# Kernel tuning notes

Measured on AMD Instinct MI355X. Metric: run time of the kernel, lower is better.

The kernel has to match this reference:

```python
import jax, jax.numpy as jnp
import numpy as np

T = 0.07          # cfg.CAP.TEMP
K = 50            # cfg.CAP.HARD_NEG_K
LOSS_WEIGHT = 0.5 # cfg.CAP.LOSS_WEIGHT
C_CAM = 8         # number of cameras
P = 2048          # pseudo-ID classes per camera bank


def setup_inputs() -> dict:
    key = jax.random.key(0)
    k1, k2, k3, k4 = jax.random.split(key, 4)
    B, D = 256, 2048
    inputs = jax.random.normal(k1, (B, D), jnp.float32)
    labels = jax.random.randint(k2, (B,), 0, P)
    cams = jax.random.randint(k3, (B,), 0, C_CAM)
    tempV = jax.random.normal(k4, (C_CAM * P, D), jnp.float32)
    tempV = tempV / jnp.linalg.norm(tempV, axis=1, keepdims=True)  # memory rows are L2-normalized
    return {"inputs": inputs, "labels": labels, "cams": cams, "tempV": tempV}


def _seg_mean_sum(vals, cams):
    # original loops over unique cams: loss += mean(vals within cam); empty cams contribute 0
    sums = jax.ops.segment_sum(vals, cams, num_segments=C_CAM)
    cnts = jax.ops.segment_sum(jnp.ones_like(vals), cams, num_segments=C_CAM)
    return jnp.sum(jnp.where(cnts > 0, sums / jnp.maximum(cnts, 1.0), 0.0))


def reference(inputs, labels, cams, tempV):
    B = inputs.shape[0]
    # cfg.CAP.NORM_FEAT
    x = inputs / jnp.linalg.norm(inputs, axis=1, keepdims=True)

    # one fused matmul against the concatenated memory; per-camera banks are contiguous P-slices
    all_logits = x @ tempV.T                      # [B, C_CAM*P]
    logits3 = all_logits.reshape(B, C_CAM, P)

    # ---- intra-camera loss: logits against the sample's own camera bank ----
    percam = jnp.take_along_axis(logits3, cams[:, None, None], axis=1)[:, 0, :] / T  # [B, P]
    lse_i = jax.scipy.special.logsumexp(percam, axis=1)
    ce = lse_i - jnp.take_along_axis(percam, labels[:, None], axis=1)[:, 0]
    loss_intra = _seg_mean_sum(ce, cams)

    # ---- inter-camera loss with hard-negative mining ----
    rows = jnp.arange(B)[:, None]
    # each ID has one centroid in every camera bank: positions label + P*cam
    ori_ind = labels[:, None] + P * jnp.arange(C_CAM)[None, :]        # [B, C_CAM]
    sims = all_logits.at[rows, ori_ind].set(-10000.0)                 # mask positives
    _, sel_ind = jax.lax.top_k(sims, K)                               # hard negatives (== sort[-K:])
    ori_logits = jnp.take_along_axis(all_logits, ori_ind, axis=1) / T  # [B, C_CAM]
    sel_logits = jnp.take_along_axis(all_logits, sel_ind, axis=1) / T  # [B, K]
    cat = jnp.concatenate([ori_logits, sel_logits], axis=1)            # [B, C_CAM+K]
    lse_c = jax.scipy.special.logsumexp(cat, axis=1)
    # target = 1/len(ori) on positives, 0 on negatives -> lse - mean(positive logits)
    loss_k = lse_c - jnp.mean(ori_logits, axis=1)
    loss_inter = LOSS_WEIGHT * _seg_mean_sum(loss_k, cams)

    return (loss_intra, loss_inter)
```

## Files before the change

kernel.cpp:

```cpp
#include <hip/hip_runtime.h>
#include <hip/hip_bf16.h>

#define BATCH 256
#define DIM   2048
#define NMEM  16384
#define PCLS  2048
#define CCAM  8
#define KSEL  50
#define T_INV 14.285714285714285714f
#define NB2   2048

typedef __bf16 bf16x8 __attribute__((ext_vector_type(8)));
typedef float  f32x4  __attribute__((ext_vector_type(4)));

static __device__ __forceinline__ unsigned int f2bf(float f) {
  unsigned int u = __float_as_uint(f);
  return (u + 0x7FFFu + ((u >> 16) & 1u)) >> 16;
}
static __device__ __forceinline__ unsigned int pk2(float lo, float hi) {
  return f2bf(lo) | (f2bf(hi) << 16);
}
static __device__ __forceinline__ int binw(float x, float lo, float scale) {
  int b = (int)((x - lo) * scale);
  return b > (NB2 - 1) ? (NB2 - 1) : b;
}

static __device__ __forceinline__ size_t pa_idx(int r, int c) {
  return (size_t)(r >> 4) * (size_t)(64 * 8 * (DIM / 32))
       + (size_t)(c >> 5) * 512
       + (size_t)(((r & 15) | (((c >> 3) & 3) << 4))) * 8
       + (size_t)(c & 7);
}

__global__ __launch_bounds__(256) void norm_cast_kernel(
    const float* __restrict__ in, unsigned short* __restrict__ xpk) {
  __shared__ float red[256];
  const int b = blockIdx.x, t = threadIdx.x;
  const float4* row = (const float4*)(in + (size_t)b * DIM);
  float4 a0 = row[t];
  float4 a1 = row[t + 256];
  float ss = a0.x*a0.x + a0.y*a0.y + a0.z*a0.z + a0.w*a0.w
           + a1.x*a1.x + a1.y*a1.y + a1.z*a1.z + a1.w*a1.w;
  red[t] = ss; __syncthreads();
  for (int s = 128; s > 0; s >>= 1) { if (t < s) red[t] += red[t + s]; __syncthreads(); }
  const float rn = rsqrtf(red[0]);
  ushort4 o0, o1;
  o0.x = (unsigned short)f2bf(a0.x*rn); o0.y = (unsigned short)f2bf(a0.y*rn);
  o0.z = (unsigned short)f2bf(a0.z*rn); o0.w = (unsigned short)f2bf(a0.w*rn);
  o1.x = (unsigned short)f2bf(a1.x*rn); o1.y = (unsigned short)f2bf(a1.y*rn);
  o1.z = (unsigned short)f2bf(a1.z*rn); o1.w = (unsigned short)f2bf(a1.w*rn);
  *(ushort4*)&xpk[pa_idx(b, 4 * t)]         = o0;
  *(ushort4*)&xpk[pa_idx(b, 4 * (t + 256))] = o1;
}

#define BN  16
#define QK  512
#define LDB 516

__global__ __launch_bounds__(256, 3) void gemm_kernel(
    const unsigned short* __restrict__ Xpk,
    const float* __restrict__ V,
    float* __restrict__ C) {
  __shared__ unsigned short Bs0[BN * LDB];
  __shared__ unsigned short Bs1[BN * LDB];
  const int t = threadIdx.x;
  const int lane = t & 63;
  const int w    = t >> 6;
  const int n0 = blockIdx.x * BN;

  const int sr = t >> 4;
  const int sc = (t & 15) * 4;
  const float* Vp = V + (size_t)(n0 + sr) * DIM + sc;
  unsigned short* Bw0 = &Bs0[sr * LDB + sc];
  unsigned short* Bw1 = &Bs1[sr * LDB + sc];

  const int fr  = lane & 15;
  const int fq8 = (lane >> 4) * 8;
  const unsigned short* Ap = Xpk + (size_t)(w * 4) * 32768 + (size_t)lane * 8;

  f32x4 acc[4];
#pragma unroll
  for (int i = 0; i < 4; i++) acc[i] = (f32x4){0.f, 0.f, 0.f, 0.f};

  {
    float4 vs[8];
#pragma unroll
    for (int g = 0; g < 8; g++) vs[g] = *(const float4*)(Vp + g * 64);
#pragma unroll
    for (int g = 0; g < 8; g++) {
      uint2 p; p.x = pk2(vs[g].x, vs[g].y); p.y = pk2(vs[g].z, vs[g].w);
      *(uint2*)(Bw0 + g * 64) = p;
    }
  }
  __syncthreads();

#pragma unroll
  for (int q = 0; q < 4; ++q) {
    const unsigned short* rb = (q & 1) ? Bs1 : Bs0;
    unsigned short*       wb = (q & 1) ? Bw0 : Bw1;
    const int kcb = q * 16;

    bf16x8 aE[4], aO[4], bE, bO;
    float4 vs[8];
    bE = *(const bf16x8*)&rb[fr * LDB + fq8];
#pragma unroll
    for (int i = 0; i < 4; ++i)
      aE[i] = *(const bf16x8*)(Ap + (size_t)i * 32768 + (size_t)kcb * 512);

#pragma unroll
    for (int j = 0; j < 16; j += 2) {
      if (q < 3)
        vs[j >> 1] = *(const float4*)(Vp + (q + 1) * QK + (j >> 1) * 64);
      bO = *(const bf16x8*)&rb[fr * LDB + (j + 1) * 32 + fq8];
#pragma unroll
      for (int i = 0; i < 4; ++i)
        aO[i] = *(const bf16x8*)(Ap + (size_t)i * 32768 + (size_t)(kcb + j + 1) * 512);
#pragma unroll
      for (int i = 0; i < 4; ++i)
        acc[i] = __builtin_amdgcn_mfma_f32_16x16x32_bf16(aE[i], bE, acc[i], 0, 0, 0);
      if (j < 14) {
        bE = *(const bf16x8*)&rb[fr * LDB + (j + 2) * 32 + fq8];
#pragma unroll
        for (int i = 0; i < 4; ++i)
          aE[i] = *(const bf16x8*)(Ap + (size_t)i * 32768 + (size_t)(kcb + j + 2) * 512);
      }
#pragma unroll
      for (int i = 0; i < 4; ++i)
        acc[i] = __builtin_amdgcn_mfma_f32_16x16x32_bf16(aO[i], bO, acc[i], 0, 0, 0);
    }

    if (q < 3) {
#pragma unroll
      for (int g = 0; g < 8; ++g) {
        uint2 p; p.x = pk2(vs[g].x, vs[g].y); p.y = pk2(vs[g].z, vs[g].w);
        *(uint2*)(wb + g * 64) = p;
      }
    }
    __syncthreads();
  }

  const int cr = (lane >> 4) * 4;
  const int cc = lane & 15;
#pragma unroll
  for (int i = 0; i < 4; i++)
#pragma unroll
    for (int r = 0; r < 4; r++)
      C[(size_t)(w * 64 + i * 16 + cr + r) * NMEM + (n0 + cc)] = acc[i][r];
}

__global__ __launch_bounds__(1024) void row_loss_kernel(
    const float* __restrict__ logits,
    const int* __restrict__ labels, const int* __restrict__ cams,
    float* __restrict__ ce_out, float* __restrict__ lossk_out) {
  __shared__ float ovs[CCAM];
  __shared__ float wredA[16], wredB[16];
  __shared__ int   hist[NB2];
  __shared__ int   pint[256];
  __shared__ float bl[512];
  __shared__ int   bcount;
  __shared__ int   bstar_s, cabove_s, totwin_s;
  __shared__ float vmax_s;

  const int b = blockIdx.x, t = threadIdx.x;
  const int lane = t & 63, wid = t >> 6;
  const int cam = cams[b], label = labels[b];
  const float* row = logits + (size_t)b * NMEM;

  if (t < CCAM) ovs[t] = row[t * PCLS + label];

  float4 rr[4];
#pragma unroll
  for (int i = 0; i < 4; i++) rr[i] = *(const float4*)(row + (size_t)(t + 1024 * i) * 4);

  float vmax = -1e30f, Si = 0.f;
#pragma unroll
  for (int i = 0; i < 4; i++) {
    const int base = (t + 1024 * i) * 4;
    const float xs[4] = {rr[i].x, rr[i].y, rr[i].z, rr[i].w};
#pragma unroll
    for (int e = 0; e < 4; e++) {
      const int n = base + e;
      const float x = xs[e];
      if ((n >> 11) == cam) Si += __expf(x * T_INV);
      if ((n & (PCLS - 1)) != label) vmax = fmaxf(vmax, x);
    }
  }
#pragma unroll
  for (int off = 32; off > 0; off >>= 1) {
    vmax = fmaxf(vmax, __shfl_down(vmax, off));
    Si  += __shfl_down(Si, off);
  }
  if (lane == 0) { wredA[wid] = vmax; wredB[wid] = Si; }
  __syncthreads();
  if (t == 0) {
    float m = -1e30f, s = 0.f;
    for (int i = 0; i < 16; i++) { m = fmaxf(m, wredA[i]); s += wredB[i]; }
    vmax_s = m;
    ce_out[b] = logf(s) - ovs[cam] * T_INV;
    bcount = 0;
  }
  __syncthreads();

  float W = 0.0625f;
  float lo = 0.f, scale = 0.f;
  for (int att = 0; att < 6; ++att) {
    __syncthreads();
    for (int i = t; i < NB2; i += 1024) hist[i] = 0;
    __syncthreads();
    lo = vmax_s - W; scale = (float)NB2 / W;
#pragma unroll
    for (int i = 0; i < 4; i++) {
      const int base = (t + 1024 * i) * 4;
      const float xs[4] = {rr[i].x, rr[i].y, rr[i].z, rr[i].w};
#pragma unroll
      for (int e = 0; e < 4; e++) {
        const int n = base + e;
        const float x = xs[e];
        if (((n & (PCLS - 1)) != label) && x >= lo)
          atomicAdd(&hist[binw(x, lo, scale)], 1);
      }
    }
    __syncthreads();
    if (t < 256) {
      int ps = 0;
#pragma unroll
      for (int i = 0; i < 8; i++) ps += hist[t * 8 + i];
      pint[t] = ps;
    }
    __syncthreads();
    if (t == 0) {
      int tot = 0;
      for (int i = 0; i < 256; i++) tot += pint[i];
      totwin_s = tot;
      if (tot >= KSEL) {
        int cum = 0, bstar = 0, cab = 0;
        for (int tc = 255; tc >= 0; tc--) {
          if (cum + pint[tc] >= KSEL) {
            for (int bi = tc * 8 + 7; bi >= tc * 8; bi--) {
              int h = hist[bi];
              if (cum + h >= KSEL) { bstar = bi; cab = cum; break; }
              cum += h;
            }
            break;
          }
          cum += pint[tc];
        }
        bstar_s = bstar; cabove_s = cab;
      }
    }
    __syncthreads();
    if (totwin_s >= KSEL) break;
    W *= 8.f;
  }
  const int bstar = bstar_s;

  float S2 = 0.f;
#pragma unroll
  for (int i = 0; i < 4; i++) {
    const int base = (t + 1024 * i) * 4;
    const float xs[4] = {rr[i].x, rr[i].y, rr[i].z, rr[i].w};
#pragma unroll
    for (int e = 0; e < 4; e++) {
      const int n = base + e;
      const float x = xs[e];
      if (((n & (PCLS - 1)) != label) && x >= lo) {
        const int bin = binw(x, lo, scale);
        if (bin > bstar) S2 += __expf(x * T_INV);
        else if (bin == bstar) {
          int p = atomicAdd(&bcount, 1);
          if (p < 512) bl[p] = x;
        }
      }
    }
  }
#pragma unroll
  for (int off = 32; off > 0; off >>= 1) S2 += __shfl_down(S2, off);
  if (lane == 0) wredB[wid] = S2;
  __syncthreads();

  if (t == 0) {
    float S2tot = 0.f;
    for (int i = 0; i < 16; i++) S2tot += wredB[i];
    const int need = KSEL - cabove_s;
    const int bc = min(bcount, 512);
    for (int r = 0; r < need; r++) {
      float mx = -1e30f; int mi = 0;
      for (int i = 0; i < bc; i++) if (bl[i] > mx) { mx = bl[i]; mi = i; }
      S2tot += __expf(mx * T_INV);
      bl[mi] = -1e30f;
    }
    float sumo = 0.f;
#pragma unroll
    for (int c = 0; c < CCAM; c++) { S2tot += __expf(ovs[c] * T_INV); sumo += ovs[c]; }
    lossk_out[b] = logf(S2tot) - (sumo * T_INV) * (1.0f / CCAM);
  }
}

__global__ __launch_bounds__(256) void finalize_kernel(
    const float* __restrict__ ce, const float* __restrict__ lossk,
    const int* __restrict__ cams, float* __restrict__ out) {
  __shared__ float ce_s[BATCH], lk_s[BATCH];
  __shared__ int   cam_s[BATCH];
  __shared__ float si[CCAM], sk[CCAM], cnt[CCAM];
  const int t = threadIdx.x;
  ce_s[t]  = ce[t];
  lk_s[t]  = lossk[t];
  cam_s[t] = cams[t];
  __syncthreads();
  if (t < CCAM) {
    float a = 0.f, b = 0.f; int n = 0;
    for (int i = 0; i < BATCH; i++) {
      if (cam_s[i] == t) { a += ce_s[i]; b += lk_s[i]; n++; }
    }
    si[t] = a; sk[t] = b; cnt[t] = (float)n;
  }
  __syncthreads();
  if (t == 0) {
    float li = 0.f, lk = 0.f;
    for (int c = 0; c < CCAM; c++) {
      if (cnt[c] > 0.f) { li += si[c] / cnt[c]; lk += sk[c] / cnt[c]; }
    }
    out[0] = li;
    out[1] = 0.5f * lk;
  }
}

extern "C" void kernel_launch(void* const* d_in, const int* in_sizes, int n_in,
                              void* d_out, int out_size, void* d_ws, size_t ws_size,
                              hipStream_t stream) {
  const float* inputs = (const float*)d_in[0];
  const int*   labels = (const int*)d_in[1];
  const int*   cams   = (const int*)d_in[2];
  const float* tempV  = (const float*)d_in[3];
  float* out = (float*)d_out;

  char* ws = (char*)d_ws;
  unsigned short* xpk = (unsigned short*)ws;
  float* logits       = (float*)(ws + (1u << 20));
  float* ce           = (float*)(ws + (1u << 20) + (16u << 20));
  float* lossk        = (float*)(ws + (1u << 20) + (16u << 20) + 1024);

  norm_cast_kernel<<<BATCH, 256, 0, stream>>>(inputs, xpk);
  gemm_kernel<<<NMEM / BN, 256, 0, stream>>>(xpk, tempV, logits);
  row_loss_kernel<<<BATCH, 1024, 0, stream>>>(logits, labels, cams, ce, lossk);
  finalize_kernel<<<1, 256, 0, stream>>>(ce, lossk, cams, out);
}
```

Before: 270.3 us.

## Retile GEMM into 128x64 blocks with 2D grid and pipelined K chunks

Result: faster. 256.8 us (-5.0%).

```diff
diff --git a/kernel.cpp b/kernel.cpp
--- a/kernel.cpp
+++ b/kernel.cpp
@@ -53,99 +53,118 @@
   *(ushort4*)&xpk[pa_idx(b, 4 * (t + 256))] = o1;
 }
 
-#define BN  16
-#define QK  512
-#define LDB 516
-
-__global__ __launch_bounds__(256, 3) void gemm_kernel(
+#define BMH 128
+#define BNW 64
+#define BKC 64
+#define NCH (DIM / BKC)
+
+__global__ __launch_bounds__(256, 2) void gemm_kernel(
     const unsigned short* __restrict__ Xpk,
     const float* __restrict__ V,
     float* __restrict__ C) {
-  __shared__ unsigned short Bs0[BN * LDB];
-  __shared__ unsigned short Bs1[BN * LDB];
-  const int t = threadIdx.x;
+  __shared__ __align__(16) unsigned short Bf[2][8][512];
+  const int t    = threadIdx.x;
   const int lane = t & 63;
-  const int w    = t >> 6;
-  const int n0 = blockIdx.x * BN;
-
-  const int sr = t >> 4;
-  const int sc = (t & 15) * 4;
-  const float* Vp = V + (size_t)(n0 + sr) * DIM + sc;
-  unsigned short* Bw0 = &Bs0[sr * LDB + sc];
-  unsigned short* Bw1 = &Bs1[sr * LDB + sc];
-
-  const int fr  = lane & 15;
-  const int fq8 = (lane >> 4) * 8;
-  const unsigned short* Ap = Xpk + (size_t)(w * 4) * 32768 + (size_t)lane * 8;
-
-  f32x4 acc[4];
-#pragma unroll
-  for (int i = 0; i < 4; i++) acc[i] = (f32x4){0.f, 0.f, 0.f, 0.f};
-
-  {
-    float4 vs[8];
-#pragma unroll
-    for (int g = 0; g < 8; g++) vs[g] = *(const float4*)(Vp + g * 64);
-#pragma unroll
-    for (int g = 0; g < 8; g++) {
-      uint2 p; p.x = pk2(vs[g].x, vs[g].y); p.y = pk2(vs[g].z, vs[g].w);
-      *(uint2*)(Bw0 + g * 64) = p;
-    }
-  }
-  __syncthreads();
-
-#pragma unroll
-  for (int q = 0; q < 4; ++q) {
-    const unsigned short* rb = (q & 1) ? Bs1 : Bs0;
-    unsigned short*       wb = (q & 1) ? Bw0 : Bw1;
-    const int kcb = q * 16;
-
-    bf16x8 aE[4], aO[4], bE, bO;
-    float4 vs[8];
-    bE = *(const bf16x8*)&rb[fr * LDB + fq8];
-#pragma unroll
-    for (int i = 0; i < 4; ++i)
-      aE[i] = *(const bf16x8*)(Ap + (size_t)i * 32768 + (size_t)kcb * 512);
-
-#pragma unroll
-    for (int j = 0; j < 16; j += 2) {
-      if (q < 3)
-        vs[j >> 1] = *(const float4*)(Vp + (q + 1) * QK + (j >> 1) * 64);
-      bO = *(const bf16x8*)&rb[fr * LDB + (j + 1) * 32 + fq8];
-#pragma unroll
-      for (int i = 0; i < 4; ++i)
-        aO[i] = *(const bf16x8*)(Ap + (size_t)i * 32768 + (size_t)(kcb + j + 1) * 512);
-#pragma unroll
-      for (int i = 0; i < 4; ++i)
-        acc[i] = __builtin_amdgcn_mfma_f32_16x16x32_bf16(aE[i], bE, acc[i], 0, 0, 0);
-      if (j < 14) {
-        bE = *(const bf16x8*)&rb[fr * LDB + (j + 2) * 32 + fq8];
-#pragma unroll
-        for (int i = 0; i < 4; ++i)
-          aE[i] = *(const bf16x8*)(Ap + (size_t)i * 32768 + (size_t)(kcb + j + 2) * 512);
-      }
-#pragma unroll
-      for (int i = 0; i < 4; ++i)
-        acc[i] = __builtin_amdgcn_mfma_f32_16x16x32_bf16(aO[i], bO, acc[i], 0, 0, 0);
-    }
-
-    if (q < 3) {
-#pragma unroll
-      for (int g = 0; g < 8; ++g) {
-        uint2 p; p.x = pk2(vs[g].x, vs[g].y); p.y = pk2(vs[g].z, vs[g].w);
-        *(uint2*)(wb + g * 64) = p;
-      }
-    }
+  const int wid  = t >> 6;
+  const int n0 = blockIdx.x * BNW;
+  const int m0 = blockIdx.y * BMH;
+
+  const int vr = t >> 2;
+  const int vq = t & 3;
+  const float* Vp = V + (size_t)(n0 + vr) * DIM + vq * 16;
+  const int wf = (vr >> 4) * 2 + (vq >> 1);
+  const int wl = 32 * (vq & 1) + (vr & 15);
+
+  const unsigned short* Apk = Xpk + (size_t)((m0 >> 4) + wid * 2) * 32768
+                                  + (size_t)lane * 8;
+
+  f32x4 acc[2][4];
+#pragma unroll
+  for (int i = 0; i < 2; i++)
+#pragma unroll
+    for (int j = 0; j < 4; j++) acc[i][j] = (f32x4){0.f, 0.f, 0.f, 0.f};
+
+  bf16x8 aE[4], aO[4];
+  float4 vE[4], vO[4];
+
+#define LOADA(SET, ch)                                                        \
+  {                                                                           \
+    const int ck_ = (ch);                                                     \
+    _Pragma("unroll")                                                         \
+    for (int i = 0; i < 2; ++i)                                               \
+      _Pragma("unroll")                                                       \
+      for (int s = 0; s < 2; ++s)                                             \
+        SET[i * 2 + s] = *(const bf16x8*)(Apk + (size_t)i * 32768             \
+                                              + (size_t)(ck_ * 2 + s) * 512); \
+  }
+#define LOADV(VS, ch)                                                         \
+  {                                                                           \
+    const int ck_ = (ch);                                                     \
+    _Pragma("unroll")                                                         \
+    for (int g = 0; g < 4; ++g)                                               \
+      VS[g] = *(const float4*)(Vp + ck_ * BKC + g * 4);                       \
+  }
+#define WRITEB(buf, VS)                                                       \
+  {                                                                           \
+    uint4 u0_, u1_;                                                           \
+    u0_.x = pk2(VS[0].x, VS[0].y); u0_.y = pk2(VS[0].z, VS[0].w);             \
+    u0_.z = pk2(VS[1].x, VS[1].y); u0_.w = pk2(VS[1].z, VS[1].w);             \
+    u1_.x = pk2(VS[2].x, VS[2].y); u1_.y = pk2(VS[2].z, VS[2].w);             \
+    u1_.z = pk2(VS[3].x, VS[3].y); u1_.w = pk2(VS[3].z, VS[3].w);             \
+    *(uint4*)&Bf[buf][wf][(size_t)wl * 8]        = u0_;                       \
+    *(uint4*)&Bf[buf][wf][(size_t)(wl + 16) * 8] = u1_;                       \
+  }
+#define COMPUTE(buf, ASET)                                                    \
+  {                                                                           \
+    _Pragma("unroll")                                                         \
+    for (int s = 0; s < 2; ++s) {                                             \
+      bf16x8 bF_[4];                                                          \
+      _Pragma("unroll")                                                       \
+      for (int j = 0; j < 4; ++j)                                             \
+        bF_[j] = *(const bf16x8*)&Bf[buf][j * 2 + s][(size_t)lane * 8];       \
+      _Pragma("unroll")                                                       \
+      for (int i = 0; i < 2; ++i)                                             \
+        _Pragma("unroll")                                                     \
+        for (int j = 0; j < 4; ++j)                                           \
+          acc[i][j] = __builtin_amdgcn_mfma_f32_16x16x32_bf16(                \
+              ASET[i * 2 + s], bF_[j], acc[i][j], 0, 0, 0);                   \
+    }                                                                         \
+  }
+
+  LOADA(aE, 0); LOADV(vE, 0);
+  WRITEB(0, vE);
+  LOADA(aO, 1); LOADV(vO, 1);
+  __syncthreads();
+
+#pragma unroll 1
+  for (int it = 0; it < NCH / 2; ++it) {
+    const int ch = 2 * it;
+    LOADV(vE, min(ch + 2, NCH - 1));
+    COMPUTE(0, aE);
+    WRITEB(1, vO);
+    LOADA(aE, min(ch + 2, NCH - 1));
+    __syncthreads();
+    LOADV(vO, min(ch + 3, NCH - 1));
+    COMPUTE(1, aO);
+    WRITEB(0, vE);
+    LOADA(aO, min(ch + 3, NCH - 1));
     __syncthreads();
   }
 
   const int cr = (lane >> 4) * 4;
   const int cc = lane & 15;
 #pragma unroll
-  for (int i = 0; i < 4; i++)
-#pragma unroll
-    for (int r = 0; r < 4; r++)
-      C[(size_t)(w * 64 + i * 16 + cr + r) * NMEM + (n0 + cc)] = acc[i][r];
+  for (int i = 0; i < 2; i++)
+#pragma unroll
+    for (int j = 0; j < 4; j++)
+#pragma unroll
+      for (int r = 0; r < 4; r++)
+        C[(size_t)(m0 + wid * 32 + i * 16 + cr + r) * NMEM + (n0 + j * 16 + cc)] =
+            acc[i][j][r];
+#undef LOADA
+#undef LOADV
+#undef WRITEB
+#undef COMPUTE
 }
 
 __global__ __launch_bounds__(1024) void row_loss_kernel(
@@ -341,7 +360,7 @@
   float* lossk        = (float*)(ws + (1u << 20) + (16u << 20) + 1024);
 
   norm_cast_kernel<<<BATCH, 256, 0, stream>>>(inputs, xpk);
-  gemm_kernel<<<NMEM / BN, 256, 0, stream>>>(xpk, tempV, logits);
+  gemm_kernel<<<dim3(NMEM / BNW, BATCH / BMH), 256, 0, stream>>>(xpk, tempV, logits);
   row_loss_kernel<<<BATCH, 1024, 0, stream>>>(logits, labels, cams, ce, lossk);
   finalize_kernel<<<1, 256, 0, stream>>>(ce, lossk, cams, out);
 }
```
